# Performance work log

Hardware: AMD Instinct MI355X
Metric: run time of the kernel (lower is better)

## Reference

```python
import jax, jax.numpy as jnp
import numpy as np

N = 50000   # nodes
E = 800000  # edges
D = 128     # embed_dim
H = 8       # num_heads
DK = D // H # d_k = 16


def _xavier(k, shape):
    lim = np.sqrt(6.0 / (shape[0] + shape[1])).astype(np.float32)
    return jax.random.uniform(k, shape, jnp.float32, -lim, lim)


def setup_inputs() -> dict:
    key = jax.random.key(0)
    ks = jax.random.split(key, 8)
    x = jax.random.normal(ks[0], (N, D), jnp.float32)
    edge_index = jax.random.randint(ks[1], (2, E), 0, N, jnp.int64)
    att_bias = jax.random.normal(ks[2], (E, H), jnp.float32)
    # Linear weights stored as [in, out] (torch stores [out, in]; math identical)
    Wq = _xavier(ks[3], (D, D)); bq = jnp.zeros((D,), jnp.float32)
    Wk = _xavier(ks[4], (D, D)); bk = jnp.zeros((D,), jnp.float32)
    Wv = _xavier(ks[5], (D, D)); bv = jnp.zeros((D,), jnp.float32)
    Wo = _xavier(ks[6], (D, D)); bo = jnp.zeros((D,), jnp.float32)
    return {"x": x, "edge_index": edge_index, "att_bias": att_bias,
            "Wq": Wq, "bq": bq, "Wk": Wk, "bk": bk,
            "Wv": Wv, "bv": bv, "Wo": Wo, "bo": bo}


def reference(x, edge_index, att_bias, Wq, bq, Wk, bk, Wv, bv, Wo, bo):
    n = x.shape[0]
    e = edge_index.shape[1]
    h = att_bias.shape[1]
    dk = Wq.shape[1] // h
    dst = edge_index[0]  # query-side node per edge (segment ids)
    src = edge_index[1]  # key/value-side node per edge

    # project on nodes (N x D GEMMs), then gather per edge -> [E, H, DK]
    q = (x @ Wq + bq)[dst].reshape(e, h, dk)
    k = (x @ Wk + bk)[src].reshape(e, h, dk)
    v = (x @ Wv + bv)[src].reshape(e, h, dk)

    scale = 1.0 / np.sqrt(dk).astype(np.float32)
    logits = scale * jnp.sum(q * k, axis=2, keepdims=True)  # [E, H, 1]
    logits = logits + att_bias[..., None]

    # segmented (scatter) softmax over edges grouped by dst node
    seg_max = jax.ops.segment_max(logits, dst, num_segments=n)   # [N, H, 1]
    ex = jnp.exp(logits - seg_max[dst])
    seg_sum = jax.ops.segment_sum(ex, dst, num_segments=n)        # [N, H, 1]
    scores = ex / seg_sum[dst]                                    # [E, H, 1]

    # weighted scatter-sum aggregation -> [N, H, DK]
    agg = jax.ops.segment_sum(scores * v, dst, num_segments=n)
    out = agg.reshape(n, h * dk) @ Wo + bo                        # [N, D]
    return out, logits
```

## Files before the change

kernel.cpp:

```cpp
#include <hip/hip_runtime.h>
#include <hip/hip_bf16.h>
#include <math.h>


typedef __bf16 bf16x8 __attribute__((ext_vector_type(8)));
typedef float  f32x4  __attribute__((ext_vector_type(4)));

__device__ __forceinline__ ushort f32_to_bf16(float f) {
    uint u = __float_as_uint(f);
    u += 0x7FFF + ((u >> 16) & 1);
    return (ushort)(u >> 16);
}
__device__ __forceinline__ uint pack_bf16x2(float a, float b) {
    return (uint)f32_to_bf16(a) | ((uint)f32_to_bf16(b) << 16);
}
__device__ __forceinline__ float bf_lo(uint w) { return __uint_as_float(w << 16); }
__device__ __forceinline__ float bf_hi(uint w) { return __uint_as_float(w & 0xFFFF0000u); }

template<int LDC, bool OUT_BF16, bool A_FP32, int NT>
__global__ __launch_bounds__(256) void gemm_mfma(
    const void* __restrict__ Av, const ushort* __restrict__ Bt,
    const float* __restrict__ bias, void* __restrict__ Cv, int M,
    const int* __restrict__ dst, const int* __restrict__ srcs,
    int* __restrict__ cnt, int2* __restrict__ pairs, int E)
{
    __shared__ uint4 As4[2048];
    __shared__ uint4 Bs4[2048];
    const int tid  = threadIdx.x;
    const int wave = tid >> 6;
    const int lane = tid & 63;
    const int qd   = lane >> 4;
    const int ln   = lane & 15;
    const int rowBase = blockIdx.x * 128;

    if (A_FP32) {
        const float4* gA = (const float4*)((const float*)Av + (size_t)rowBase * 128);
        #pragma unroll
        for (int i = 0; i < 16; ++i) {
            int c32 = tid + i * 256;
            int r   = c32 >> 5;
            float4 v = make_float4(0.f, 0.f, 0.f, 0.f);
            if (rowBase + r < M) v = gA[c32];
            ushort4 hh;
            hh.x = f32_to_bf16(v.x); hh.y = f32_to_bf16(v.y);
            hh.z = f32_to_bf16(v.z); hh.w = f32_to_bf16(v.w);
            int c16 = c32 >> 1;
            int lc  = (c16 & ~15) | ((c16 ^ (c16 >> 4)) & 15);
            ((ushort4*)As4)[lc * 2 + (c32 & 1)] = hh;
        }
    } else {
        const uint4* gA = (const uint4*)((const ushort*)Av + (size_t)rowBase * 128);
        #pragma unroll
        for (int i = 0; i < 8; ++i) {
            int c  = tid + i * 256;
            int lc = (c & ~15) | ((c ^ (c >> 4)) & 15);
            As4[lc] = gA[c];
        }
    }

    #pragma unroll
    for (int by = 0; by < NT; ++by) {
        const int colBase = by * 128;
        if (by > 0) __syncthreads();
        const uint4* gB = (const uint4*)(Bt + (size_t)colBase * 128);
        #pragma unroll
        for (int i = 0; i < 8; ++i) {
            int c  = tid + i * 256;
            int lc = (c & ~15) | ((c ^ (c >> 4)) & 15);
            Bs4[lc] = gB[c];
        }
        __syncthreads();

        f32x4 acc[2][8];
        #pragma unroll
        for (int i = 0; i < 2; ++i)
            #pragma unroll
            for (int j = 0; j < 8; ++j)
                acc[i][j] = (f32x4){0.f, 0.f, 0.f, 0.f};

        const int m0 = wave * 32;
        #pragma unroll
        for (int ks = 0; ks < 4; ++ks) {
            const int kc = ks * 4 + qd;
            bf16x8 a0 = *((const bf16x8*)&As4[(m0 +      ln) * 16 + (kc ^ ln)]);
            bf16x8 a1 = *((const bf16x8*)&As4[(m0 + 16 + ln) * 16 + (kc ^ ln)]);
            #pragma unroll
            for (int j = 0; j < 8; ++j) {
                bf16x8 b = *((const bf16x8*)&Bs4[(j * 16 + ln) * 16 + (kc ^ ln)]);
                acc[0][j] = __builtin_amdgcn_mfma_f32_16x16x32_bf16(b, a0, acc[0][j], 0, 0, 0);
                acc[1][j] = __builtin_amdgcn_mfma_f32_16x16x32_bf16(b, a1, acc[1][j], 0, 0, 0);
            }
        }

        #pragma unroll
        for (int i = 0; i < 2; ++i) {
            int gr = rowBase + m0 + i * 16 + ln;
            if (gr < M) {
                #pragma unroll
                for (int j = 0; j < 8; ++j) {
                    int coln = colBase + j * 16 + qd * 4;
                    float4 b4 = *((const float4*)(bias + coln));
                    float v0 = acc[i][j][0] + b4.x;
                    float v1 = acc[i][j][1] + b4.y;
                    float v2 = acc[i][j][2] + b4.z;
                    float v3 = acc[i][j][3] + b4.w;
                    if (OUT_BF16) {
                        uint2 o;
                        o.x = pack_bf16x2(v0, v1);
                        o.y = pack_bf16x2(v2, v3);
                        *((uint2*)((ushort*)Cv + (size_t)gr * LDC + coln)) = o;
                    } else {
                        float4 o = make_float4(v0, v1, v2, v3);
                        *((float4*)((float*)Cv + (size_t)gr * LDC + coln)) = o;
                    }
                }
            }
        }
    }

    if (E > 0) {
        const int gsz = gridDim.x * 256;
        for (int e = blockIdx.x * 256 + tid; e < E; e += gsz) {
            int d  = dst[e];
            int rk = atomicAdd(&cnt[d], 1);
            if (rk < 64) pairs[((size_t)d << 6) + rk] = make_int2(srcs[e], e);
        }
    }
}

__global__ __launch_bounds__(256) void prep_kernel(
    const float* __restrict__ Wq, const float* __restrict__ Wk,
    const float* __restrict__ Wv, const float* __restrict__ bq,
    const float* __restrict__ bk, const float* __restrict__ bv,
    const float* __restrict__ Wo,
    ushort* __restrict__ WcatT, float* __restrict__ bcatI, ushort* __restrict__ WoT,
    int* __restrict__ cnt, int N, int GSZ)
{
    const int gid = blockIdx.x * 256 + threadIdx.x;

    for (int i = gid; i < N; i += GSZ) cnt[i] = 0;

    const int WTOT = 384 * 128 + 384 + 128 * 128;
    for (int idx = gid; idx < WTOT; idx += GSZ) {
        if (idx < 384 * 128) {
            int jj = idx >> 7, k = idx & 127;
            const float* W; int c;
            if (jj < 128)      { W = Wq; c = jj; }
            else if (jj < 256) { W = Wk; c = jj - 128; }
            else               { W = Wv; c = jj - 256; }
            WcatT[idx] = f32_to_bf16(W[k * 128 + c]);
        } else if (idx < 384 * 128 + 384) {
            int jj = idx - 384 * 128;
            float b;
            if (jj < 128)      b = bq[jj];
            else if (jj < 256) b = bk[jj - 128];
            else               b = bv[jj - 256];
            bcatI[jj] = b;
        } else {
            int t = idx - (384 * 128 + 384);
            int n = t >> 7, k = t & 127;
            WoT[t] = f32_to_bf16(Wo[k * 128 + n]);
        }
    }
}

__global__ __launch_bounds__(256) void attn_kernel(
    const ushort* __restrict__ Cb, const int* __restrict__ deg,
    const int2* __restrict__ pairs, const float* __restrict__ att_bias,
    float* __restrict__ logits_out, ushort* __restrict__ aggb, int N)
{
    const int wv   = threadIdx.x >> 6;
    const int lane = threadIdx.x & 63;
    const int node = blockIdx.x * 4 + wv;
    if (node >= N) return;
    const int eg   = lane >> 4;
    const int r    = lane & 15;
    const int h    = r >> 1;
    const int half = lane & 1;

    const char* cb = (const char*)Cb;

    uint4 qw = *((const uint4*)(cb + (size_t)node * 768) + r);
    const float q0 = bf_lo(qw.x), q1 = bf_hi(qw.x);
    const float q2 = bf_lo(qw.y), q3 = bf_hi(qw.y);
    const float q4 = bf_lo(qw.z), q5 = bf_hi(qw.z);
    const float q6 = bf_lo(qw.w), q7 = bf_hi(qw.w);

    const int dg = min(deg[node], 64);

    float l = 0.f;
    float a0 = 0.f, a1 = 0.f, a2 = 0.f, a3 = 0.f;
    float a4 = 0.f, a5 = 0.f, a6 = 0.f, a7 = 0.f;

    if (dg > 0) {
        int gidx = (node << 6) + ((lane < dg) ? lane : (dg - 1));
        int2 se = pairs[gidx];
        int regSrc = se.x;
        int regEid = se.y;

        uint4 kwA, vwA; float bbA; int eidA; bool validA;
        uint4 kwB, vwB; float bbB; int eidB; bool validB = false;

        {
            int idxr = eg;
            validA = idxr < dg;
            int idxc = validA ? idxr : (dg - 1);
            int srcn = __shfl(regSrc, idxc);
            eidA = __shfl(regEid, idxc);
            const char* kv = cb + (size_t)((uint)srcn * 768u);
            kwA = *((const uint4*)(kv + 256) + r);
            vwA = *((const uint4*)(kv + 512) + r);
            bbA = att_bias[eidA * 8 + h];
        }

        for (int g = 0; g < dg; g += 8) {
            if (g + 4 < dg) {
                int idxr = g + 4 + eg;
                validB = idxr < dg;
                int idxc = validB ? idxr : (dg - 1);
                int srcn = __shfl(regSrc, idxc);
                eidB = __shfl(regEid, idxc);
                const char* kv = cb + (size_t)((uint)srcn * 768u);
                kwB = *((const uint4*)(kv + 256) + r);
                vwB = *((const uint4*)(kv + 512) + r);
                bbB = att_bias[eidB * 8 + h];
            }
            {
                float p = q0 * bf_lo(kwA.x) + q1 * bf_hi(kwA.x)
                        + q2 * bf_lo(kwA.y) + q3 * bf_hi(kwA.y)
                        + q4 * bf_lo(kwA.z) + q5 * bf_hi(kwA.z)
                        + q6 * bf_lo(kwA.w) + q7 * bf_hi(kwA.w);
                p += __shfl_xor(p, 1);
                float logit = p * 0.25f + bbA;
                if (validA && half == 0) logits_out[eidA * 8 + h] = logit;
                float pe = validA ? __expf(logit) : 0.f;
                l += pe;
                a0 = fmaf(pe, bf_lo(vwA.x), a0); a1 = fmaf(pe, bf_hi(vwA.x), a1);
                a2 = fmaf(pe, bf_lo(vwA.y), a2); a3 = fmaf(pe, bf_hi(vwA.y), a3);
                a4 = fmaf(pe, bf_lo(vwA.z), a4); a5 = fmaf(pe, bf_hi(vwA.z), a5);
                a6 = fmaf(pe, bf_lo(vwA.w), a6); a7 = fmaf(pe, bf_hi(vwA.w), a7);
            }
            if (g + 8 < dg) {
                int idxr = g + 8 + eg;
                validA = idxr < dg;
                int idxc = validA ? idxr : (dg - 1);
                int srcn = __shfl(regSrc, idxc);
                eidA = __shfl(regEid, idxc);
                const char* kv = cb + (size_t)((uint)srcn * 768u);
                kwA = *((const uint4*)(kv + 256) + r);
                vwA = *((const uint4*)(kv + 512) + r);
                bbA = att_bias[eidA * 8 + h];
            }
            if (g + 4 < dg) {
                float p = q0 * bf_lo(kwB.x) + q1 * bf_hi(kwB.x)
                        + q2 * bf_lo(kwB.y) + q3 * bf_hi(kwB.y)
                        + q4 * bf_lo(kwB.z) + q5 * bf_hi(kwB.z)
                        + q6 * bf_lo(kwB.w) + q7 * bf_hi(kwB.w);
                p += __shfl_xor(p, 1);
                float logit = p * 0.25f + bbB;
                if (validB && half == 0) logits_out[eidB * 8 + h] = logit;
                float pe = validB ? __expf(logit) : 0.f;
                l += pe;
                a0 = fmaf(pe, bf_lo(vwB.x), a0); a1 = fmaf(pe, bf_hi(vwB.x), a1);
                a2 = fmaf(pe, bf_lo(vwB.y), a2); a3 = fmaf(pe, bf_hi(vwB.y), a3);
                a4 = fmaf(pe, bf_lo(vwB.z), a4); a5 = fmaf(pe, bf_hi(vwB.z), a5);
                a6 = fmaf(pe, bf_lo(vwB.w), a6); a7 = fmaf(pe, bf_hi(vwB.w), a7);
            }
        }
    }

    #pragma unroll
    for (int m = 16; m <= 32; m <<= 1) {
        l  += __shfl_xor(l, m);
        a0 += __shfl_xor(a0, m); a1 += __shfl_xor(a1, m);
        a2 += __shfl_xor(a2, m); a3 += __shfl_xor(a3, m);
        a4 += __shfl_xor(a4, m); a5 += __shfl_xor(a5, m);
        a6 += __shfl_xor(a6, m); a7 += __shfl_xor(a7, m);
    }
    float inv = (l > 0.f) ? (1.f / l) : 0.f;
    if (eg == 0) {
        uint4 o;
        o.x = pack_bf16x2(a0 * inv, a1 * inv);
        o.y = pack_bf16x2(a2 * inv, a3 * inv);
        o.z = pack_bf16x2(a4 * inv, a5 * inv);
        o.w = pack_bf16x2(a6 * inv, a7 * inv);
        ((uint4*)(aggb + (size_t)node * 128))[r] = o;
    }
}

extern "C" void kernel_launch(void* const* d_in, const int* in_sizes, int n_in,
                              void* d_out, int out_size, void* d_ws, size_t ws_size,
                              hipStream_t stream)
{
    const float* x        = (const float*)d_in[0];
    const int*   ei       = (const int*)d_in[1];
    const float* att_bias = (const float*)d_in[2];
    const float* Wq = (const float*)d_in[3];  const float* bq = (const float*)d_in[4];
    const float* Wk = (const float*)d_in[5];  const float* bk = (const float*)d_in[6];
    const float* Wv = (const float*)d_in[7];  const float* bv = (const float*)d_in[8];
    const float* Wo = (const float*)d_in[9];  const float* bo = (const float*)d_in[10];

    const int N = in_sizes[0] / 128;
    const int E = in_sizes[1] / 2;

    float* out    = (float*)d_out;
    float* logits = out + (size_t)N * 128;

    char* ws = (char*)d_ws;
    size_t o = 0;
    auto alloc = [&](size_t bytes) -> char* {
        char* p = ws + o;
        o = (o + bytes + 255) & ~(size_t)255;
        return p;
    };
    const int Mpad = ((N + 127) / 128) * 128;
    ushort* Cb    = (ushort*)alloc((size_t)N * 384 * 2);
    ushort* aggb  = (ushort*)alloc((size_t)Mpad * 128 * 2);
    ushort* WcatT = (ushort*)alloc((size_t)384 * 128 * 2);
    float*  bcatI = (float*)alloc(384 * 4);
    ushort* WoT   = (ushort*)alloc((size_t)128 * 128 * 2);
    int*    cnt   = (int*)alloc((size_t)N * 4);
    int2*   pairs = (int2*)alloc((size_t)N * 64 * 8);

    const int MB = (N + 127) / 128;

    const int PREP_BLOCKS = 512;
    prep_kernel<<<PREP_BLOCKS, 256, 0, stream>>>(
        Wq, Wk, Wv, bq, bk, bv, Wo, WcatT, bcatI, WoT, cnt,
        N, PREP_BLOCKS * 256);

    gemm_mfma<384, true, true, 3><<<MB, 256, 0, stream>>>(
        x, WcatT, bcatI, Cb, N, ei, ei + E, cnt, pairs, E);

    attn_kernel<<<(N + 3) / 4, 256, 0, stream>>>(Cb, cnt, pairs, att_bias,
                                                 logits, aggb, N);

    gemm_mfma<128, false, false, 1><<<MB, 256, 0, stream>>>(
        aggb, WoT, bo, out, N, nullptr, nullptr, nullptr, nullptr, 0);
}
```

Baseline: 260.5 us.

## Fuse output projection into attention kernel via per-block MFMA

The attention kernel now processes 8 nodes per 512-thread block, writes the normalized aggregated vectors into shared memory, and then each wave computes a 16-column slice of the Wo projection with bf16 MFMA, adding the bias and writing fp32 output directly. This removes the separate output GEMM launch and the global round trip of the aggregated bf16 buffer. In exchange each block does a padded 16-row MFMA with only 8 valid rows, which wastes half the MFMA work. It also re-reads WoT from global/L2 in every block and adds block-wide synchronization.

```diff
diff --git a/kernel.cpp b/kernel.cpp
--- a/kernel.cpp
+++ b/kernel.cpp
@@ -164,84 +164,51 @@
     }
 }
 
-__global__ __launch_bounds__(256) void attn_kernel(
+__global__ __launch_bounds__(512) void attn_kernel(
     const ushort* __restrict__ Cb, const int* __restrict__ deg,
     const int2* __restrict__ pairs, const float* __restrict__ att_bias,
-    float* __restrict__ logits_out, ushort* __restrict__ aggb, int N)
+    const ushort* __restrict__ WoT, const float* __restrict__ bo,
+    float* __restrict__ logits_out, float* __restrict__ out, int N)
 {
-    const int wv   = threadIdx.x >> 6;
-    const int lane = threadIdx.x & 63;
-    const int node = blockIdx.x * 4 + wv;
-    if (node >= N) return;
+    __shared__ ushort aggB[16 * 136];
+    const int tid  = threadIdx.x;
+    const int wv   = tid >> 6;
+    const int lane = tid & 63;
+    const int node = blockIdx.x * 8 + wv;
     const int eg   = lane >> 4;
     const int r    = lane & 15;
     const int h    = r >> 1;
     const int half = lane & 1;
 
+    for (int i = tid; i < 16 * 136; i += 512) aggB[i] = 0;
+    __syncthreads();
+
     const char* cb = (const char*)Cb;
 
-    uint4 qw = *((const uint4*)(cb + (size_t)node * 768) + r);
-    const float q0 = bf_lo(qw.x), q1 = bf_hi(qw.x);
-    const float q2 = bf_lo(qw.y), q3 = bf_hi(qw.y);
-    const float q4 = bf_lo(qw.z), q5 = bf_hi(qw.z);
-    const float q6 = bf_lo(qw.w), q7 = bf_hi(qw.w);
-
-    const int dg = min(deg[node], 64);
-
-    float l = 0.f;
-    float a0 = 0.f, a1 = 0.f, a2 = 0.f, a3 = 0.f;
-    float a4 = 0.f, a5 = 0.f, a6 = 0.f, a7 = 0.f;
-
-    if (dg > 0) {
-        int gidx = (node << 6) + ((lane < dg) ? lane : (dg - 1));
-        int2 se = pairs[gidx];
-        int regSrc = se.x;
-        int regEid = se.y;
-
-        uint4 kwA, vwA; float bbA; int eidA; bool validA;
-        uint4 kwB, vwB; float bbB; int eidB; bool validB = false;
-
-        {
-            int idxr = eg;
-            validA = idxr < dg;
-            int idxc = validA ? idxr : (dg - 1);
-            int srcn = __shfl(regSrc, idxc);
-            eidA = __shfl(regEid, idxc);
-            const char* kv = cb + (size_t)((uint)srcn * 768u);
-            kwA = *((const uint4*)(kv + 256) + r);
-            vwA = *((const uint4*)(kv + 512) + r);
-            bbA = att_bias[eidA * 8 + h];
-        }
-
-        for (int g = 0; g < dg; g += 8) {
-            if (g + 4 < dg) {
-                int idxr = g + 4 + eg;
-                validB = idxr < dg;
-                int idxc = validB ? idxr : (dg - 1);
-                int srcn = __shfl(regSrc, idxc);
-                eidB = __shfl(regEid, idxc);
-                const char* kv = cb + (size_t)((uint)srcn * 768u);
-                kwB = *((const uint4*)(kv + 256) + r);
-                vwB = *((const uint4*)(kv + 512) + r);
-                bbB = att_bias[eidB * 8 + h];
-            }
+    if (node < N) {
+        uint4 qw = *((const uint4*)(cb + (size_t)node * 768) + r);
+        const float q0 = bf_lo(qw.x), q1 = bf_hi(qw.x);
+        const float q2 = bf_lo(qw.y), q3 = bf_hi(qw.y);
+        const float q4 = bf_lo(qw.z), q5 = bf_hi(qw.z);
+        const float q6 = bf_lo(qw.w), q7 = bf_hi(qw.w);
+
+        const int dg = min(deg[node], 64);
+
+        float l = 0.f;
+        float a0 = 0.f, a1 = 0.f, a2 = 0.f, a3 = 0.f;
+        float a4 = 0.f, a5 = 0.f, a6 = 0.f, a7 = 0.f;
+
+        if (dg > 0) {
+            int gidx = (node << 6) + ((lane < dg) ? lane : (dg - 1));
+            int2 se = pairs[gidx];
+            int regSrc = se.x;
+            int regEid = se.y;
+
+            uint4 kwA, vwA; float bbA; int eidA; bool validA;
+            uint4 kwB, vwB; float bbB; int eidB; bool validB = false;
+
             {
-                float p = q0 * bf_lo(kwA.x) + q1 * bf_hi(kwA.x)
-                        + q2 * bf_lo(kwA.y) + q3 * bf_hi(kwA.y)
-                        + q4 * bf_lo(kwA.z) + q5 * bf_hi(kwA.z)
-                        + q6 * bf_lo(kwA.w) + q7 * bf_hi(kwA.w);
-                p += __shfl_xor(p, 1);
-                float logit = p * 0.25f + bbA;
-                if (validA && half == 0) logits_out[eidA * 8 + h] = logit;
-                float pe = validA ? __expf(logit) : 0.f;
-                l += pe;
-                a0 = fmaf(pe, bf_lo(vwA.x), a0); a1 = fmaf(pe, bf_hi(vwA.x), a1);
-                a2 = fmaf(pe, bf_lo(vwA.y), a2); a3 = fmaf(pe, bf_hi(vwA.y), a3);
-                a4 = fmaf(pe, bf_lo(vwA.z), a4); a5 = fmaf(pe, bf_hi(vwA.z), a5);
-                a6 = fmaf(pe, bf_lo(vwA.w), a6); a7 = fmaf(pe, bf_hi(vwA.w), a7);
-            }
-            if (g + 8 < dg) {
-                int idxr = g + 8 + eg;
+                int idxr = eg;
                 validA = idxr < dg;
                 int idxc = validA ? idxr : (dg - 1);
                 int srcn = __shfl(regSrc, idxc);
@@ -251,40 +218,103 @@
                 vwA = *((const uint4*)(kv + 512) + r);
                 bbA = att_bias[eidA * 8 + h];
             }
-            if (g + 4 < dg) {
-                float p = q0 * bf_lo(kwB.x) + q1 * bf_hi(kwB.x)
-                        + q2 * bf_lo(kwB.y) + q3 * bf_hi(kwB.y)
-                        + q4 * bf_lo(kwB.z) + q5 * bf_hi(kwB.z)
-                        + q6 * bf_lo(kwB.w) + q7 * bf_hi(kwB.w);
-                p += __shfl_xor(p, 1);
-                float logit = p * 0.25f + bbB;
-                if (validB && half == 0) logits_out[eidB * 8 + h] = logit;
-                float pe = validB ? __expf(logit) : 0.f;
-                l += pe;
-                a0 = fmaf(pe, bf_lo(vwB.x), a0); a1 = fmaf(pe, bf_hi(vwB.x), a1);
-                a2 = fmaf(pe, bf_lo(vwB.y), a2); a3 = fmaf(pe, bf_hi(vwB.y), a3);
-                a4 = fmaf(pe, bf_lo(vwB.z), a4); a5 = fmaf(pe, bf_hi(vwB.z), a5);
-                a6 = fmaf(pe, bf_lo(vwB.w), a6); a7 = fmaf(pe, bf_hi(vwB.w), a7);
+
+            for (int g = 0; g < dg; g += 8) {
+                if (g + 4 < dg) {
+                    int idxr = g + 4 + eg;
+                    validB = idxr < dg;
+                    int idxc = validB ? idxr : (dg - 1);
+                    int srcn = __shfl(regSrc, idxc);
+                    eidB = __shfl(regEid, idxc);
+                    const char* kv = cb + (size_t)((uint)srcn * 768u);
+                    kwB = *((const uint4*)(kv + 256) + r);
+                    vwB = *((const uint4*)(kv + 512) + r);
+                    bbB = att_bias[eidB * 8 + h];
+                }
+                {
+                    float p = q0 * bf_lo(kwA.x) + q1 * bf_hi(kwA.x)
+                            + q2 * bf_lo(kwA.y) + q3 * bf_hi(kwA.y)
+                            + q4 * bf_lo(kwA.z) + q5 * bf_hi(kwA.z)
+                            + q6 * bf_lo(kwA.w) + q7 * bf_hi(kwA.w);
+                    p += __shfl_xor(p, 1);
+                    float logit = p * 0.25f + bbA;
+                    if (validA && half == 0) logits_out[eidA * 8 + h] = logit;
+                    float pe = validA ? __expf(logit) : 0.f;
+                    l += pe;
+                    a0 = fmaf(pe, bf_lo(vwA.x), a0); a1 = fmaf(pe, bf_hi(vwA.x), a1);
+                    a2 = fmaf(pe, bf_lo(vwA.y), a2); a3 = fmaf(pe, bf_hi(vwA.y), a3);
+                    a4 = fmaf(pe, bf_lo(vwA.z), a4); a5 = fmaf(pe, bf_hi(vwA.z), a5);
+                    a6 = fmaf(pe, bf_lo(vwA.w), a6); a7 = fmaf(pe, bf_hi(vwA.w), a7);
+                }
+                if (g + 8 < dg) {
+                    int idxr = g + 8 + eg;
+                    validA = idxr < dg;
+                    int idxc = validA ? idxr : (dg - 1);
+                    int srcn = __shfl(regSrc, idxc);
+                    eidA = __shfl(regEid, idxc);
+                    const char* kv = cb + (size_t)((uint)srcn * 768u);
+                    kwA = *((const uint4*)(kv + 256) + r);
+                    vwA = *((const uint4*)(kv + 512) + r);
+                    bbA = att_bias[eidA * 8 + h];
+                }
+                if (g + 4 < dg) {
+                    float p = q0 * bf_lo(kwB.x) + q1 * bf_hi(kwB.x)
+                            + q2 * bf_lo(kwB.y) + q3 * bf_hi(kwB.y)
+                            + q4 * bf_lo(kwB.z) + q5 * bf_hi(kwB.z)
+                            + q6 * bf_lo(kwB.w) + q7 * bf_hi(kwB.w);
+                    p += __shfl_xor(p, 1);
+                    float logit = p * 0.25f + bbB;
+                    if (validB && half == 0) logits_out[eidB * 8 + h] = logit;
+                    float pe = validB ? __expf(logit) : 0.f;
+                    l += pe;
+                    a0 = fmaf(pe, bf_lo(vwB.x), a0); a1 = fmaf(pe, bf_hi(vwB.x), a1);
+                    a2 = fmaf(pe, bf_lo(vwB.y), a2); a3 = fmaf(pe, bf_hi(vwB.y), a3);
+                    a4 = fmaf(pe, bf_lo(vwB.z), a4); a5 = fmaf(pe, bf_hi(vwB.z), a5);
+                    a6 = fmaf(pe, bf_lo(vwB.w), a6); a7 = fmaf(pe, bf_hi(vwB.w), a7);
+                }
             }
         }
-    }
-
-    #pragma unroll
-    for (int m = 16; m <= 32; m <<= 1) {
-        l  += __shfl_xor(l, m);
-        a0 += __shfl_xor(a0, m); a1 += __shfl_xor(a1, m);
-        a2 += __shfl_xor(a2, m); a3 += __shfl_xor(a3, m);
-        a4 += __shfl_xor(a4, m); a5 += __shfl_xor(a5, m);
-        a6 += __shfl_xor(a6, m); a7 += __shfl_xor(a7, m);
-    }
-    float inv = (l > 0.f) ? (1.f / l) : 0.f;
-    if (eg == 0) {
-        uint4 o;
-        o.x = pack_bf16x2(a0 * inv, a1 * inv);
-        o.y = pack_bf16x2(a2 * inv, a3 * inv);
-        o.z = pack_bf16x2(a4 * inv, a5 * inv);
-        o.w = pack_bf16x2(a6 * inv, a7 * inv);
-        ((uint4*)(aggb + (size_t)node * 128))[r] = o;
+
+        #pragma unroll
+        for (int m = 16; m <= 32; m <<= 1) {
+            l  += __shfl_xor(l, m);
+            a0 += __shfl_xor(a0, m); a1 += __shfl_xor(a1, m);
+            a2 += __shfl_xor(a2, m); a3 += __shfl_xor(a3, m);
+            a4 += __shfl_xor(a4, m); a5 += __shfl_xor(a5, m);
+            a6 += __shfl_xor(a6, m); a7 += __shfl_xor(a7, m);
+        }
+        float inv = (l > 0.f) ? (1.f / l) : 0.f;
+        if (eg == 0) {
+            uint4 o;
+            o.x = pack_bf16x2(a0 * inv, a1 * inv);
+            o.y = pack_bf16x2(a2 * inv, a3 * inv);
+            o.z = pack_bf16x2(a4 * inv, a5 * inv);
+            o.w = pack_bf16x2(a6 * inv, a7 * inv);
+            *((uint4*)&aggB[wv * 136 + r * 8]) = o;
+        }
+    }
+    __syncthreads();
+
+    {
+        const int qd = lane >> 4;
+        const int ln = lane & 15;
+        f32x4 acc = (f32x4){0.f, 0.f, 0.f, 0.f};
+        const uint4* Wg = (const uint4*)WoT;
+        #pragma unroll
+        for (int ks = 0; ks < 4; ++ks) {
+            const int kc = ks * 4 + qd;
+            bf16x8 a = *((const bf16x8*)&aggB[ln * 136 + kc * 8]);
+            bf16x8 b = *((const bf16x8*)&Wg[wv * 256 + ln * 16 + ks * 4 + qd]);
+            acc = __builtin_amdgcn_mfma_f32_16x16x32_bf16(b, a, acc, 0, 0, 0);
+        }
+        const int gr = blockIdx.x * 8 + ln;
+        if (ln < 8 && gr < N) {
+            const int coln = wv * 16 + qd * 4;
+            float4 b4 = *((const float4*)(bo + coln));
+            float4 o = make_float4(acc[0] + b4.x, acc[1] + b4.y,
+                                   acc[2] + b4.z, acc[3] + b4.w);
+            *((float4*)(out + (size_t)gr * 128 + coln)) = o;
+        }
     }
 }
 
@@ -313,9 +343,7 @@
         o = (o + bytes + 255) & ~(size_t)255;
         return p;
     };
-    const int Mpad = ((N + 127) / 128) * 128;
     ushort* Cb    = (ushort*)alloc((size_t)N * 384 * 2);
-    ushort* aggb  = (ushort*)alloc((size_t)Mpad * 128 * 2);
     ushort* WcatT = (ushort*)alloc((size_t)384 * 128 * 2);
     float*  bcatI = (float*)alloc(384 * 4);
     ushort* WoT   = (ushort*)alloc((size_t)128 * 128 * 2);
@@ -332,9 +360,6 @@
     gemm_mfma<384, true, true, 3><<<MB, 256, 0, stream>>>(
         x, WcatT, bcatI, Cb, N, ei, ei + E, cnt, pairs, E);
 
-    attn_kernel<<<(N + 3) / 4, 256, 0, stream>>>(Cb, cnt, pairs, att_bias,
-                                                 logits, aggb, N);
-
-    gemm_mfma<128, false, false, 1><<<MB, 256, 0, stream>>>(
-        aggb, WoT, bo, out, N, nullptr, nullptr, nullptr, nullptr, 0);
-}
+    attn_kernel<<<(N + 7) / 8, 512, 0, stream>>>(Cb, cnt, pairs, att_bias,
+                                                 WoT, bo, logits, out, N);
+}
```

Result: no change. 260.6 us (+0.0%).
